# Performance work log

Hardware: AMD Instinct MI355X
Metric: run time of the kernel (lower is better)

## Reference

```python
import jax, jax.numpy as jnp
import numpy as np

B, L, NV = 16, 512, 64
D = 512
PATCH_LEN, STRIDE, PADDING = 16, 8, 8
N_PATCH = (L - PATCH_LEN) // STRIDE + 2  # 64
PRED = 192
MEM = 8192
TOPK = 8
NHEAD = 4
NORM_CONST = 0.4
HEAD_NF = D * N_PATCH


def _pos_emb(n, d):
    pos = np.arange(n)[:, None].astype(np.float32)
    div = np.exp(np.arange(0, d, 2).astype(np.float32) * (-np.log(10000.0) / d))
    pe = np.zeros((n, d), np.float32)
    pe[:, 0::2] = np.sin(pos * div)
    pe[:, 1::2] = np.cos(pos * div)
    return jnp.asarray(pe)

POS = _pos_emb(N_PATCH, D)


def gelu(x):
    return jax.nn.gelu(x, approximate=False)  # torch nn.GELU default = exact erf


def setup_inputs() -> dict:
    key = jax.random.key(0)
    ks = jax.random.split(key, 16)
    s = lambda i, shape, scale=0.02: jax.random.normal(ks[i], shape, jnp.float32) * scale
    return dict(
        x_enc=jax.random.normal(ks[0], (B, L, NV), jnp.float32),
        W_val=s(1, (PATCH_LEN, D), 0.05),
        mem_bank=s(2, (MEM, D), 1.0),
        W_m1=s(3, (D, 2 * D)), b_m1=jnp.zeros((2 * D,), jnp.float32),
        W_m2=s(4, (2 * D, D)), b_m2=jnp.zeros((D,), jnp.float32),
        W_q=s(5, (D, D)), b_q=jnp.zeros((D,), jnp.float32),
        W_k=s(6, (D, D)), b_k=jnp.zeros((D,), jnp.float32),
        W_v=s(7, (D, D)), b_v=jnp.zeros((D,), jnp.float32),
        W_o=s(8, (D, D)), b_o=jnp.zeros((D,), jnp.float32),
        W_g1=s(9, (2 * D, D)), b_g1=jnp.zeros((D,), jnp.float32),
        W_g2=s(10, (D, 2)), b_g2=jnp.zeros((2,), jnp.float32),
        W_h=s(11, (HEAD_NF, PRED)), b_h=jnp.zeros((PRED,), jnp.float32),
        W_f1=s(12, (PRED, 2 * PRED)), b_f1=jnp.zeros((2 * PRED,), jnp.float32),
        W_f2=s(13, (2 * PRED, PRED)), b_f2=jnp.zeros((PRED,), jnp.float32),
    )


def reference(x_enc, W_val, mem_bank, W_m1, b_m1, W_m2, b_m2,
              W_q, b_q, W_k, b_k, W_v, b_v, W_o, b_o,
              W_g1, b_g1, W_g2, b_g2, W_h, b_h, W_f1, b_f1, W_f2, b_f2):
    # instance normalization over the time axis (means detached in torch)
    means = jax.lax.stop_gradient(jnp.mean(x_enc, axis=1, keepdims=True))
    xc = x_enc - means
    stdev = jnp.sqrt(jnp.var(xc, axis=1, keepdims=True) + 1e-5) / NORM_CONST
    x = xc / stdev                                              # [B, L, NV]

    # patch embedding: replication pad at end, unfold, linear + sinusoidal pos
    xt = jnp.transpose(x, (0, 2, 1))                            # [B, NV, L]
    xt = jnp.concatenate([xt, jnp.repeat(xt[..., -1:], PADDING, axis=-1)], axis=-1)
    win = (jnp.arange(N_PATCH) * STRIDE)[:, None] + jnp.arange(PATCH_LEN)  # [N, P]
    patches = xt[..., win].reshape(B * NV, N_PATCH, PATCH_LEN)  # [BN, N, P]
    emb = patches @ W_val + POS                                 # [BN, N, D]

    # local memory: mean-pooled query -> matmul similarity -> top-k gather -> MLP
    qflat = jnp.mean(emb, axis=1)                               # [BN, D]
    sim = qflat @ mem_bank.T                                    # [BN, MEM]
    _, idx = jax.lax.top_k(sim, TOPK)                           # [BN, K]
    retr = mem_bank[idx]                                        # [BN, K, D]
    h = gelu(retr @ W_m1 + b_m1) @ W_m2 + b_m2
    local = jnp.mean(h, axis=1, keepdims=True) + emb            # [BN, N, D]

    # global memory: multihead self-attention (4 heads, batch_first)
    dh = D // NHEAD
    heads = lambda t: t.reshape(B * NV, N_PATCH, NHEAD, dh).transpose(0, 2, 1, 3)
    q = heads(emb @ W_q + b_q)
    k = heads(emb @ W_k + b_k)
    v = heads(emb @ W_v + b_v)
    att = jax.nn.softmax(jnp.einsum('bhqd,bhkd->bhqk', q, k) / jnp.sqrt(jnp.float32(dh)), axis=-1)
    glob = jnp.einsum('bhqk,bhkd->bhqd', att, v).transpose(0, 2, 1, 3).reshape(B * NV, N_PATCH, D)
    glob = glob @ W_o + b_o                                     # [BN, N, D]

    # gated fusion of local/global memory
    comb = jnp.concatenate([local, glob], axis=-1)              # [BN, N, 2D]
    gate = jax.nn.softmax(gelu(comb @ W_g1 + b_g1) @ W_g2 + b_g2, axis=-1)
    mem = gate[..., 0:1] * local + gate[..., 1:2] * glob        # [BN, N, D]

    # flatten -> memory head -> fusion layer with residual
    flat = mem.reshape(B * NV, HEAD_NF)
    mh = (flat @ W_h + b_h).reshape(B, NV, PRED)
    pred = gelu(gelu(mh @ W_f1 + b_f1) @ W_f2 + b_f2) + mh
    pred = jnp.transpose(pred, (0, 2, 1))                       # [B, PRED, NV]

    # denormalize
    return pred * stdev + means
```

## Files before the change

kernel.cpp:

```cpp
#include <hip/hip_runtime.h>
#include <stdint.h>

#define DEV __device__ __forceinline__

typedef uint16_t u16;
typedef __bf16 bf16x8 __attribute__((ext_vector_type(8)));
typedef float f32x4 __attribute__((ext_vector_type(4)));
typedef u16 u16x8 __attribute__((ext_vector_type(8)));

DEV float bf2f(u16 v) { return __uint_as_float(((uint32_t)v) << 16); }
DEV u16 f2bf(float f) {
  uint32_t u = __float_as_uint(f);
  u += 0x7fffu + ((u >> 16) & 1u);
  return (u16)(u >> 16);
}
DEV float gelu_f(float x) { return 0.5f * x * (1.0f + erff(x * 0.7071067811865475f)); }

DEV void gload_lds16(const u16* g, u16* l) {
  __builtin_amdgcn_global_load_lds(
      (const __attribute__((address_space(1))) void*)g,
      (__attribute__((address_space(3))) void*)l, 16, 0, 0);
}

struct __align__(16) Scratch {
  float POSb[64 * 512];
  float meanv[1024];
  float stdv[1024];
  float mh[1024 * 192];
  int idxB[8192];
  float qflat[1024 * 512];
  float gatel[65536 * 2];
  float bqkv[1536];
  u16 hmeanB[1024 * 512];
  u16 gmeanB[1024 * 1024];
  u16 WqkvT[1536 * 512];
  u16 WoT[512 * 512];
  u16 Wm1T[1024 * 512];
  u16 Wm2T[512 * 1024];
  u16 Wg1T[512 * 1024];
  u16 WhT[256 * 32768];
  u16 memdupB[8192 * 1536];
  u16 embh[65536 * 512];
  u16 locglob[65536 * 1024];
  u16 obuf[65536 * 512];
  u16 qkvb[65536 * 1536];
};
__device__ Scratch g_s;

__global__ __launch_bounds__(256) void zerof_kernel(float* __restrict__ p, int n) {
  int t = blockIdx.x * 256 + threadIdx.x;
  if (t < n) p[t] = 0.f;
}
__global__ __launch_bounds__(256) void zerou8_kernel(u16* __restrict__ p, int n8) {
  int t = blockIdx.x * 256 + threadIdx.x;
  if (t < n8) *(u16x8*)(p + (long)t * 8) = (u16x8)0;
}
__global__ __launch_bounds__(256) void biasqkv_kernel(const float* __restrict__ bq,
                                                      const float* __restrict__ bk,
                                                      const float* __restrict__ bv,
                                                      float* __restrict__ o) {
  int t = blockIdx.x * 256 + threadIdx.x;
  o[t] = t < 512 ? bq[t] : (t < 1024 ? bk[t - 512] : bv[t - 1024]);
}

__global__ __launch_bounds__(256) void pos_kernel(float* __restrict__ POS) {
  int n = blockIdx.x;
  int i = threadIdx.x;
  float div = expf((float)(2 * i) * (-9.210340371976184f / 512.0f));
  float arg = (float)n * div;
  POS[n * 512 + 2 * i] = sinf(arg);
  POS[n * 512 + 2 * i + 1] = cosf(arg);
}

__global__ __launch_bounds__(256) void stats_kernel(const float* __restrict__ x_enc,
                                                    float* __restrict__ meanv,
                                                    float* __restrict__ stdv) {
  int b = blockIdx.x;
  int v = threadIdx.x & 63;
  int g = threadIdx.x >> 6;
  float s = 0.f, s2 = 0.f;
  for (int l = g; l < 512; l += 4) {
    float x = x_enc[((long)b * 512 + l) * 64 + v];
    s += x; s2 += x * x;
  }
  __shared__ float sh[2][4][64];
  sh[0][g][v] = s; sh[1][g][v] = s2;
  __syncthreads();
  if (g == 0) {
    s = sh[0][0][v] + sh[0][1][v] + sh[0][2][v] + sh[0][3][v];
    s2 = sh[1][0][v] + sh[1][1][v] + sh[1][2][v] + sh[1][3][v];
    float mu = s * (1.f / 512.f);
    float var = s2 * (1.f / 512.f) - mu * mu;
    meanv[b * 64 + v] = mu;
    stdv[b * 64 + v] = sqrtf(var + 1e-5f) * 2.5f;
  }
}

__global__ __launch_bounds__(256) void transpose_kernel(const float* __restrict__ in,
                                                        u16* __restrict__ out, int R, int C) {
  __shared__ u16 t[32][33];
  int bx = blockIdx.x * 32;
  int by = blockIdx.y * 32;
  int tx = threadIdx.x & 31, ty = threadIdx.x >> 5;
  for (int i = ty; i < 32; i += 8) t[i][tx] = f2bf(in[(long)(by + i) * C + bx + tx]);
  __syncthreads();
  for (int i = ty; i < 32; i += 8) out[(long)(bx + i) * R + by + tx] = t[tx][i];
}

__global__ __launch_bounds__(256) void emb_kernel(const float* __restrict__ x_enc,
                                                  const float* __restrict__ W_val,
                                                  const float* __restrict__ POS,
                                                  const float* __restrict__ meanv,
                                                  const float* __restrict__ stdv,
                                                  u16* __restrict__ embh,
                                                  u16* __restrict__ qsC) {
  int bn = blockIdx.x;
  int b = bn >> 6, v = bn & 63;
  int tid = threadIdx.x;
  __shared__ __align__(16) float wv[16 * 512];
  __shared__ __align__(16) float pt[64 * 16];
  for (int i = tid; i < 8192; i += 256) wv[i] = W_val[i];
  float mu = meanv[bn];
  float inv = 1.f / stdv[bn];
  for (int i = tid; i < 1024; i += 256) {
    int n = i >> 4, p = i & 15;
    int l = n * 8 + p; if (l > 511) l = 511;
    pt[i] = (x_enc[((long)b * 512 + l) * 64 + v] - mu) * inv;
  }
  __syncthreads();
  float qs0 = 0.f, qs1 = 0.f;
  int d0 = tid, d1 = tid + 256;
  for (int n = 0; n < 64; ++n) {
    float a0 = POS[n * 512 + d0], a1 = POS[n * 512 + d1];
#pragma unroll
    for (int p = 0; p < 16; ++p) {
      float pv = pt[n * 16 + p];
      a0 += pv * wv[p * 512 + d0];
      a1 += pv * wv[p * 512 + d1];
    }
    long base = ((long)bn * 64 + n) * 512;
    embh[base + d0] = f2bf(a0);
    embh[base + d1] = f2bf(a1);
    qs0 += a0; qs1 += a1;
  }
  float q0 = qs0 * (1.f / 64.f), q1 = qs1 * (1.f / 64.f);
  u16 h0 = f2bf(q0), l0 = f2bf(q0 - bf2f(h0));
  u16 h1 = f2bf(q1), l1 = f2bf(q1 - bf2f(h1));
  long qb = (long)bn * 1536;
  qsC[qb + d0] = h0; qsC[qb + 512 + d0] = l0; qsC[qb + 1024 + d0] = h0;
  qsC[qb + d1] = h1; qsC[qb + 512 + d1] = l1; qsC[qb + 1024 + d1] = h1;
}

__global__ __launch_bounds__(256) void memdup_kernel(const float* __restrict__ mb,
                                                     u16* __restrict__ md) {
  int t = blockIdx.x * 256 + threadIdx.x;
  int n = t >> 6, k8 = (t & 63) * 8;
  const float* src = mb + (long)n * 512 + k8;
  u16x8 hi, lo;
#pragma unroll
  for (int z = 0; z < 8; ++z) {
    float m = src[z];
    u16 h = f2bf(m);
    hi[z] = h;
    lo[z] = f2bf(m - bf2f(h));
  }
  long base = (long)n * 1536 + k8;
  *(u16x8*)(md + base) = hi;
  *(u16x8*)(md + base + 512) = hi;
  *(u16x8*)(md + base + 1024) = lo;
}

template <int EPI>
__global__ __launch_bounds__(256) void gemm_db(const u16* __restrict__ Ag,
                                               const u16* __restrict__ Bt,
                                               const float* __restrict__ bias,
                                               void* __restrict__ C,
                                               const float* __restrict__ W_g2,
                                               float* __restrict__ gatel,
                                               int lda, int ldb, int K, int Nreal, int ldc,
                                               int nT, long zstride) {
  __shared__ __align__(16) u16 smem[4 * 128 * 64];
  const int tid = threadIdx.x;
  const int id = blockIdx.x;
  const int xcd = id & 7;
  const int kk = id >> 3;
  const long bm = (long)((kk / nT) * 8 + xcd) * 128;
  const long bnn = (long)(kk % nT) * 128;
  const long koff = (long)blockIdx.z * (long)K;
  const int lane = tid & 63;
  const int w = tid >> 6;
  const int wm = (w & 1) * 64;
  const int wn = (w >> 1) * 64;
  const int r16 = lane & 15;
  const int q4 = lane >> 4;

  f32x4 acc[4][4] = {};

  const u16* ap[4];
  const u16* bp[4];
  int ao[4], bo[4];
#pragma unroll
  for (int j = 0; j < 4; ++j) {
    int cid = (j * 4 + w) * 64 + lane;
    int r = cid >> 3;
    int g = (cid & 7) ^ (r & 7);
    ap[j] = Ag + (bm + r) * lda + koff + g * 8;
    bp[j] = Bt + (bnn + r) * ldb + koff + g * 8;
    ao[j] = cid * 8;
    bo[j] = 8192 + cid * 8;
  }

#pragma unroll
  for (int j = 0; j < 4; ++j) gload_lds16(ap[j], smem + ao[j]);
#pragma unroll
  for (int j = 0; j < 4; ++j) gload_lds16(bp[j], smem + bo[j]);

  const int nsteps = K >> 6;
  for (int s = 0; s < nsteps; ++s) {
    const int cur = s & 1;
    u16* buf = smem + cur * 16384;
    if (s + 1 < nsteps) {
      u16* nb = smem + (cur ^ 1) * 16384;
      const int k1 = (s + 1) << 6;
#pragma unroll
      for (int j = 0; j < 4; ++j) gload_lds16(ap[j] + k1, nb + ao[j]);
#pragma unroll
      for (int j = 0; j < 4; ++j) gload_lds16(bp[j] + k1, nb + bo[j]);
      asm volatile("s_waitcnt vmcnt(8)" ::: "memory");
    } else {
      asm volatile("s_waitcnt vmcnt(0)" ::: "memory");
    }
    __builtin_amdgcn_sched_barrier(0);
    __builtin_amdgcn_s_barrier();
    __builtin_amdgcn_sched_barrier(0);
    u16* As = buf;
    u16* Bs = buf + 8192;
#pragma unroll
    for (int sub = 0; sub < 2; ++sub) {
      const int gg = q4 + sub * 4;
      bf16x8 av[4], bv[4];
#pragma unroll
      for (int i = 0; i < 4; ++i) {
        int r = wm + i * 16 + r16;
        av[i] = *reinterpret_cast<const bf16x8*>(As + (r * 8 + (gg ^ (r & 7))) * 8);
      }
#pragma unroll
      for (int j2 = 0; j2 < 4; ++j2) {
        int r = wn + j2 * 16 + r16;
        bv[j2] = *reinterpret_cast<const bf16x8*>(Bs + (r * 8 + (gg ^ (r & 7))) * 8);
      }
#pragma unroll
      for (int i = 0; i < 4; ++i)
#pragma unroll
        for (int j2 = 0; j2 < 4; ++j2)
          acc[i][j2] = __builtin_amdgcn_mfma_f32_16x16x32_bf16(av[i], bv[j2], acc[i][j2], 0, 0, 0);
    }
    __builtin_amdgcn_sched_barrier(0);
    __builtin_amdgcn_s_barrier();
    __builtin_amdgcn_sched_barrier(0);
  }

  if (EPI == 3) {
    float* Cz = (float*)C + (long)blockIdx.z * zstride;
    float* epf = (float*)smem + w * 2048;
#pragma unroll
    for (int half = 0; half < 2; ++half) {
#pragma unroll
      for (int i = 0; i < 2; ++i)
#pragma unroll
        for (int j = 0; j < 4; ++j)
#pragma unroll
          for (int r = 0; r < 4; ++r)
            epf[(i * 16 + q4 * 4 + r) * 64 + j * 16 + r16] = acc[half * 2 + i][j][r];
      __syncthreads();
#pragma unroll
      for (int v2 = 0; v2 < 8; ++v2) {
        int idx = v2 * 64 + lane;
        int row = idx >> 4, c4 = (idx & 15) * 4;
        f32x4 vec = *(const f32x4*)(epf + row * 64 + c4);
        long grow = bm + wm + half * 32 + row;
        int gcol = (int)bnn + wn + c4;
        if (gcol < Nreal) *(f32x4*)(Cz + grow * (long)ldc + gcol) = vec;
      }
      __syncthreads();
    }
  } else if (EPI == 4) {
    float bcol[4], w0[4], w1[4];
#pragma unroll
    for (int j = 0; j < 4; ++j) {
      int gc = (int)bnn + wn + j * 16 + r16;
      bcol[j] = bias[gc];
      w0[j] = W_g2[gc * 2];
      w1[j] = W_g2[gc * 2 + 1];
    }
#pragma unroll
    for (int i = 0; i < 4; ++i)
#pragma unroll
      for (int r = 0; r < 4; ++r) {
        float a0 = 0.f, a1 = 0.f;
#pragma unroll
        for (int j = 0; j < 4; ++j) {
          float h = gelu_f(acc[i][j][r] + bcol[j]);
          a0 += h * w0[j];
          a1 += h * w1[j];
        }
#pragma unroll
        for (int off = 1; off < 16; off <<= 1) {
          a0 += __shfl_xor(a0, off);
          a1 += __shfl_xor(a1, off);
        }
        if (r16 == 0) {
          long row = bm + wm + i * 16 + q4 * 4 + r;
          atomicAdd(&gatel[row * 2], a0);
          atomicAdd(&gatel[row * 2 + 1], a1);
        }
      }
  } else {
    u16* ep = smem + w * 2304;
    float bcol[4];
#pragma unroll
    for (int j = 0; j < 4; ++j) bcol[j] = bias[bnn + wn + j * 16 + r16];
#pragma unroll
    for (int half = 0; half < 2; ++half) {
#pragma unroll
      for (int i = 0; i < 2; ++i)
#pragma unroll
        for (int j = 0; j < 4; ++j)
#pragma unroll
          for (int r = 0; r < 4; ++r) {
            float v = acc[half * 2 + i][j][r] + bcol[j];
            if (EPI == 1) v = gelu_f(v);
            ep[(i * 16 + q4 * 4 + r) * 72 + j * 16 + r16] = f2bf(v);
          }
      __syncthreads();
#pragma unroll
      for (int v2 = 0; v2 < 4; ++v2) {
        int row = v2 * 8 + (lane >> 3);
        int c8 = (lane & 7) * 8;
        u16x8 vec = *(const u16x8*)(ep + row * 72 + c8);
        long grow = bm + wm + half * 32 + row;
        int gcol = (int)bnn + wn + c8;
        if (gcol < Nreal) *(u16x8*)((u16*)C + grow * (long)ldc + gcol) = vec;
      }
      __syncthreads();
    }
  }
}

DEV bool better(float v1, int i1, float v2, int i2) {
  return v1 > v2 || (v1 == v2 && i1 < i2);
}
__global__ __launch_bounds__(256) void topk_kernel(const float* __restrict__ sim,
                                                   int* __restrict__ idxout) {
  const int bn = blockIdx.x;
  const int tid = threadIdx.x;
  const float* row = sim + (long)bn * 8192;
  float bv[8]; int bi[8];
#pragma unroll
  for (int r = 0; r < 8; ++r) { bv[r] = -3.0e38f; bi[r] = 0x7fffffff; }
  for (int n = tid; n < 8192; n += 256) {
    float v = row[n];
    if (better(v, n, bv[7], bi[7])) {
      bv[7] = v; bi[7] = n;
      for (int r = 7; r > 0; --r) {
        if (!better(bv[r], bi[r], bv[r - 1], bi[r - 1])) break;
        float tv = bv[r]; bv[r] = bv[r - 1]; bv[r - 1] = tv;
        int ti = bi[r]; bi[r] = bi[r - 1]; bi[r - 1] = ti;
      }
    }
  }
  __shared__ float lv[256 * 8];
  __shared__ int li[256 * 8];
#pragma unroll
  for (int r = 0; r < 8; ++r) { lv[tid * 8 + r] = bv[r]; li[tid * 8 + r] = bi[r]; }
  __syncthreads();
  for (int step = 128; step >= 1; step >>= 1) {
    if (tid < step) {
      float av[8], xv[8]; int ai[8], xi[8];
#pragma unroll
      for (int r = 0; r < 8; ++r) {
        av[r] = lv[tid * 8 + r]; ai[r] = li[tid * 8 + r];
        xv[r] = lv[(tid + step) * 8 + r]; xi[r] = li[(tid + step) * 8 + r];
      }
      int ia = 0, ib = 0;
      float mv[8]; int mi[8];
#pragma unroll
      for (int r = 0; r < 8; ++r) {
        if (better(av[ia], ai[ia], xv[ib], xi[ib])) { mv[r] = av[ia]; mi[r] = ai[ia]; ++ia; }
        else { mv[r] = xv[ib]; mi[r] = xi[ib]; ++ib; }
      }
#pragma unroll
      for (int r = 0; r < 8; ++r) { lv[tid * 8 + r] = mv[r]; li[tid * 8 + r] = mi[r]; }
    }
    __syncthreads();
  }
  if (tid < 8) idxout[bn * 8 + tid] = li[tid];
}

__global__ __launch_bounds__(256) void gather_kernel(const float* __restrict__ mb,
                                                     const int* __restrict__ idx,
                                                     u16* __restrict__ retrB) {
  int t = blockIdx.x * 256 + threadIdx.x;
  int m = t >> 6;
  int c8 = (t & 63) * 8;
  long r = idx[m];
  if (r < 0) r = 0;
  if (r > 8191) r = 8191;
  const float* src = mb + r * 512 + c8;
  u16x8 o;
#pragma unroll
  for (int z = 0; z < 8; ++z) o[z] = f2bf(src[z]);
  *(u16x8*)(retrB + (long)m * 512 + c8) = o;
}

__global__ __launch_bounds__(256) void gmean_kernel(const u16* __restrict__ hid,
                                                    u16* __restrict__ gmeanB) {
  int t = blockIdx.x * 256 + threadIdx.x;
  int bn = t >> 7, j8 = (t & 127) * 8;
  float s[8] = {};
#pragma unroll
  for (int k = 0; k < 8; ++k) {
    u16x8 v = *(const u16x8*)(hid + (long)(bn * 8 + k) * 1024 + j8);
#pragma unroll
    for (int z = 0; z < 8; ++z) s[z] += bf2f(v[z]);
  }
  u16x8 o;
#pragma unroll
  for (int z = 0; z < 8; ++z) o[z] = f2bf(s[z] * 0.125f);
  *(u16x8*)(gmeanB + (long)bn * 1024 + j8) = o;
}

__global__ __launch_bounds__(256) void attn_kernel(const u16* __restrict__ qkvb,
                                                   u16* __restrict__ obuf) {
  __shared__ __align__(16) u16 smem[26752];
  u16* Qs = smem;
  u16* Ks = smem + 8704;
  float* ss = (float*)(smem + 8704);
  u16* ps = smem;
  u16* Os = smem;
  u16* Vb = smem + 17408;
  float* red = (float*)(smem + 25728);
  const int bn = blockIdx.x, h = blockIdx.y;
  const int tid = threadIdx.x;
  const int lane = tid & 63, w = tid >> 6;
  const int r16 = lane & 15, q4 = lane >> 4;
  const long base = (long)bn * 64 * 1536 + h * 128;

  for (int c = tid; c < 1024; c += 256) {
    int r = c >> 4, c8 = (c & 15) * 8;
    u16x8 vq = *(const u16x8*)(qkvb + base + (long)r * 1536 + c8);
    u16x8 vk = *(const u16x8*)(qkvb + base + (long)r * 1536 + 512 + c8);
    u16x8 vv = *(const u16x8*)(qkvb + base + (long)r * 1536 + 1024 + c8);
    *(u16x8*)(Qs + r * 136 + c8) = vq;
    *(u16x8*)(Ks + r * 136 + c8) = vk;
    int kt = r >> 5, q4t = (r >> 3) & 3, e = r & 7;
    int nt = c8 >> 4, rb = c8 & 15;
    int vbase = (nt * 2 + kt) * 520 + (q4t * 16 + rb) * 8 + e;
#pragma unroll
    for (int z = 0; z < 8; ++z) Vb[vbase + z * 8] = vv[z];
  }
  __syncthreads();

  const int m0 = w * 16;
  f32x4 accS[4] = {};
#pragma unroll
  for (int k0 = 0; k0 < 128; k0 += 32) {
    bf16x8 av = *(const bf16x8*)(Qs + (m0 + r16) * 136 + k0 + q4 * 8);
#pragma unroll
    for (int j = 0; j < 4; ++j) {
      bf16x8 bvf = *(const bf16x8*)(Ks + (j * 16 + r16) * 136 + k0 + q4 * 8);
      accS[j] = __builtin_amdgcn_mfma_f32_16x16x32_bf16(av, bvf, accS[j], 0, 0, 0);
    }
  }
  __syncthreads();
  const float scale = 0.08838834764831845f;
#pragma unroll
  for (int j = 0; j < 4; ++j)
#pragma unroll
    for (int r = 0; r < 4; ++r)
      ss[(m0 + q4 * 4 + r) * 66 + j * 16 + r16] = accS[j][r] * scale;
  __syncthreads();

  {
    int r = tid >> 2, p = tid & 3;
    float* row = ss + r * 66 + p * 16;
    float mx = -3.0e38f;
#pragma unroll
    for (int c2 = 0; c2 < 16; ++c2) mx = fmaxf(mx, row[c2]);
    red[r * 4 + p] = mx;
    __syncthreads();
    float m4 = fmaxf(fmaxf(red[r * 4], red[r * 4 + 1]),
                     fmaxf(red[r * 4 + 2], red[r * 4 + 3]));
    float s = 0.f;
#pragma unroll
    for (int c2 = 0; c2 < 16; ++c2) {
      float e = expf(row[c2] - m4);
      row[c2] = e;
      s += e;
    }
    red[256 + r * 4 + p] = s;
    __syncthreads();
    float inv = 1.f / (red[256 + r * 4] + red[256 + r * 4 + 1] +
                       red[256 + r * 4 + 2] + red[256 + r * 4 + 3]);
    u16x8 o0, o1;
#pragma unroll
    for (int z = 0; z < 8; ++z) {
      o0[z] = f2bf(row[z] * inv);
      o1[z] = f2bf(row[8 + z] * inv);
    }
    *(u16x8*)(ps + r * 72 + p * 16) = o0;
    *(u16x8*)(ps + r * 72 + p * 16 + 8) = o1;
  }
  __syncthreads();

  bf16x8 av0 = *(const bf16x8*)(ps + (m0 + r16) * 72 + q4 * 8);
  bf16x8 av1 = *(const bf16x8*)(ps + (m0 + r16) * 72 + 32 + q4 * 8);
  __syncthreads();
#pragma unroll
  for (int nt = 0; nt < 8; ++nt) {
    f32x4 accO = {};
    bf16x8 bv0 = *(const bf16x8*)(Vb + (nt * 2 + 0) * 520 + lane * 8);
    bf16x8 bv1 = *(const bf16x8*)(Vb + (nt * 2 + 1) * 520 + lane * 8);
    accO = __builtin_amdgcn_mfma_f32_16x16x32_bf16(av0, bv0, accO, 0, 0, 0);
    accO = __builtin_amdgcn_mfma_f32_16x16x32_bf16(av1, bv1, accO, 0, 0, 0);
#pragma unroll
    for (int r = 0; r < 4; ++r) {
      int i = m0 + q4 * 4 + r;
      int col = nt * 16 + r16;
      Os[i * 128 + (col ^ (q4 << 4))] = f2bf(accO[r]);
    }
  }
  __syncthreads();
#pragma unroll
  for (int z = 0; z < 4; ++z) {
    int idx = z * 256 + tid;
    int row = idx >> 4, c8 = (idx & 15) * 8;
    int c8s = c8 ^ (((row >> 2) & 3) << 4);
    u16x8 vec = *(const u16x8*)(Os + row * 128 + c8s);
    *(u16x8*)(obuf + ((long)bn * 64 + row) * 512 + h * 128 + c8) = vec;
  }
}

__global__ __launch_bounds__(256) void local_kernel(const u16* __restrict__ embh,
                                                    const u16* __restrict__ hmeanB,
                                                    u16* __restrict__ locglob) {
  long t = (long)blockIdx.x * 256 + threadIdx.x;
  long e8 = t * 8;
  long m = e8 >> 9;
  int d = (int)(e8 & 511);
  int bn = (int)(m >> 6);
  u16x8 a = *(const u16x8*)(embh + e8);
  u16x8 b = *(const u16x8*)(hmeanB + (long)bn * 512 + d);
  u16x8 o;
#pragma unroll
  for (int z = 0; z < 8; ++z) o[z] = f2bf(bf2f(a[z]) + bf2f(b[z]));
  *(u16x8*)(locglob + m * 1024 + d) = o;
}

__global__ __launch_bounds__(256) void memc_kernel(u16* __restrict__ embh,
                                                   const u16* __restrict__ locglob,
                                                   const float* __restrict__ gatel,
                                                   const float* __restrict__ b_g2) {
  long t = (long)blockIdx.x * 256 + threadIdx.x;
  long e8 = t * 8;
  long m = e8 >> 9;
  int d = (int)(e8 & 511);
  float l0 = gatel[m * 2] + b_g2[0];
  float l1 = gatel[m * 2 + 1] + b_g2[1];
  float mx = fmaxf(l0, l1);
  float e0 = expf(l0 - mx), e1 = expf(l1 - mx);
  float inv = 1.f / (e0 + e1);
  float g0 = e0 * inv, g1 = e1 * inv;
  u16x8 loc = *(const u16x8*)(locglob + m * 1024 + d);
  u16x8 gl = *(const u16x8*)(locglob + m * 1024 + 512 + d);
  u16x8 o;
#pragma unroll
  for (int z = 0; z < 8; ++z) o[z] = f2bf(g0 * bf2f(loc[z]) + g1 * bf2f(gl[z]));
  *(u16x8*)(embh + e8) = o;
}

__global__ __launch_bounds__(256) void fusion_kernel(const float* __restrict__ mh16,
                                                     const float* __restrict__ b_h,
                                                     const float* __restrict__ W_f1,
                                                     const float* __restrict__ b_f1,
                                                     const float* __restrict__ W_f2,
                                                     const float* __restrict__ b_f2,
                                                     const float* __restrict__ meanv,
                                                     const float* __restrict__ stdv,
                                                     float* __restrict__ out) {
  int bn = blockIdx.x;
  int tid = threadIdx.x;
  __shared__ float mrow[192];
  __shared__ float h1[384];
  if (tid < 192) {
    float a = b_h[tid];
#pragma unroll
    for (int z = 0; z < 16; ++z) a += mh16[(long)z * 196608 + (long)bn * 192 + tid];
    mrow[tid] = a;
  }
  __syncthreads();
  for (int j = tid; j < 384; j += 256) {
    float a = b_f1[j];
    for (int i = 0; i < 192; ++i) a += mrow[i] * W_f1[i * 384 + j];
    h1[j] = gelu_f(a);
  }
  __syncthreads();
  if (tid < 192) {
    float a = b_f2[tid];
    for (int j = 0; j < 384; ++j) a += h1[j] * W_f2[j * 192 + tid];
    float o = gelu_f(a) + mrow[tid];
    int b = bn >> 6, v = bn & 63;
    out[((long)b * 192 + tid) * 64 + v] = o * stdv[bn] + meanv[bn];
  }
}

extern "C" void kernel_launch(void* const* d_in, const int* in_sizes, int n_in,
                              void* d_out, int out_size, void* d_ws, size_t ws_size,
                              hipStream_t stream) {
  (void)in_sizes; (void)n_in; (void)out_size; (void)d_ws; (void)ws_size;
  const float* x_enc = (const float*)d_in[0];
  const float* W_val = (const float*)d_in[1];
  const float* mem_bank = (const float*)d_in[2];
  const float* W_m1 = (const float*)d_in[3];
  const float* b_m1 = (const float*)d_in[4];
  const float* W_m2 = (const float*)d_in[5];
  const float* b_m2 = (const float*)d_in[6];
  const float* W_q = (const float*)d_in[7];
  const float* b_q = (const float*)d_in[8];
  const float* W_k = (const float*)d_in[9];
  const float* b_k = (const float*)d_in[10];
  const float* W_v = (const float*)d_in[11];
  const float* b_v = (const float*)d_in[12];
  const float* W_o = (const float*)d_in[13];
  const float* b_o = (const float*)d_in[14];
  const float* W_g1 = (const float*)d_in[15];
  const float* b_g1 = (const float*)d_in[16];
  const float* W_g2 = (const float*)d_in[17];
  const float* b_g2 = (const float*)d_in[18];
  const float* W_h = (const float*)d_in[19];
  const float* b_h = (const float*)d_in[20];
  const float* W_f1 = (const float*)d_in[21];
  const float* b_f1 = (const float*)d_in[22];
  const float* W_f2 = (const float*)d_in[23];
  const float* b_f2 = (const float*)d_in[24];

  void* sp = nullptr;
  hipGetSymbolAddress(&sp, HIP_SYMBOL(g_s));
  Scratch* S = (Scratch*)sp;
  float* simB = (float*)S->qkvb;
  u16* qsC = S->qkvb + (size_t)16 * 1024 * 1024;
  u16* retrB = S->qkvb + (size_t)18 * 1024 * 1024;
  u16* hiddenB = S->qkvb + (size_t)24 * 1024 * 1024;
  float* mh16 = (float*)S->qkvb;

  pos_kernel<<<64, 256, 0, stream>>>(S->POSb);
  stats_kernel<<<16, 256, 0, stream>>>(x_enc, S->meanv, S->stdv);
  zerof_kernel<<<512, 256, 0, stream>>>(S->gatel, 65536 * 2);
  zerou8_kernel<<<1024, 256, 0, stream>>>(S->WhT + (size_t)192 * 32768, 64 * 32768 / 8);
  biasqkv_kernel<<<6, 256, 0, stream>>>(b_q, b_k, b_v, S->bqkv);
  transpose_kernel<<<dim3(16, 16), 256, 0, stream>>>(W_q, S->WqkvT, 512, 512);
  transpose_kernel<<<dim3(16, 16), 256, 0, stream>>>(W_k, S->WqkvT + 512 * 512, 512, 512);
  transpose_kernel<<<dim3(16, 16), 256, 0, stream>>>(W_v, S->WqkvT + 2 * 512 * 512, 512, 512);
  transpose_kernel<<<dim3(16, 16), 256, 0, stream>>>(W_o, S->WoT, 512, 512);
  transpose_kernel<<<dim3(32, 16), 256, 0, stream>>>(W_m1, S->Wm1T, 512, 1024);
  transpose_kernel<<<dim3(16, 32), 256, 0, stream>>>(W_m2, S->Wm2T, 1024, 512);
  transpose_kernel<<<dim3(16, 32), 256, 0, stream>>>(W_g1, S->Wg1T, 1024, 512);
  transpose_kernel<<<dim3(6, 1024), 256, 0, stream>>>(W_h, S->WhT, 32768, 192);
  memdup_kernel<<<2048, 256, 0, stream>>>(mem_bank, S->memdupB);

  emb_kernel<<<1024, 256, 0, stream>>>(x_enc, W_val, S->POSb, S->meanv, S->stdv,
                                       S->embh, qsC);
  gemm_db<3><<<512, 256, 0, stream>>>(qsC, S->memdupB, nullptr, simB, nullptr, nullptr,
                                      1536, 1536, 1536, 8192, 8192, 64, 0L);
  topk_kernel<<<1024, 256, 0, stream>>>(simB, S->idxB);
  gather_kernel<<<2048, 256, 0, stream>>>(mem_bank, S->idxB, retrB);
  gemm_db<1><<<512, 256, 0, stream>>>(retrB, S->Wm1T, b_m1, hiddenB, nullptr, nullptr,
                                      512, 512, 512, 1024, 1024, 8, 0L);
  gmean_kernel<<<512, 256, 0, stream>>>(hiddenB, S->gmeanB);
  gemm_db<0><<<32, 256, 0, stream>>>(S->gmeanB, S->Wm2T, b_m2, S->hmeanB, nullptr, nullptr,
                                     1024, 1024, 1024, 512, 512, 4, 0L);
  gemm_db<0><<<6144, 256, 0, stream>>>(S->embh, S->WqkvT, S->bqkv, S->qkvb, nullptr, nullptr,
                                       512, 512, 512, 1536, 1536, 12, 0L);
  local_kernel<<<16384, 256, 0, stream>>>(S->embh, S->hmeanB, S->locglob);
  attn_kernel<<<dim3(1024, 4), 256, 0, stream>>>(S->qkvb, S->obuf);
  gemm_db<0><<<2048, 256, 0, stream>>>(S->obuf, S->WoT, b_o, S->locglob + 512, nullptr, nullptr,
                                       512, 512, 512, 512, 1024, 4, 0L);
  gemm_db<4><<<2048, 256, 0, stream>>>(S->locglob, S->Wg1T, b_g1, nullptr,
                                       W_g2, S->gatel, 1024, 1024, 1024, 512, 0, 4, 0L);
  memc_kernel<<<16384, 256, 0, stream>>>(S->embh, S->locglob, S->gatel, b_g2);
  gemm_db<3><<<dim3(16, 1, 16), 256, 0, stream>>>(S->embh, S->WhT, nullptr, mh16,
                                                  nullptr, nullptr,
                                                  32768, 32768, 2048, 192, 192, 2,
                                                  196608L);
  fusion_kernel<<<1024, 256, 0, stream>>>(mh16, b_h, W_f1, b_f1, W_f2, b_f2,
                                          S->meanv, S->stdv, (float*)d_out);
}
```

Before: 933.9 us.

## Merge prep kernels, fuse gather into topk, split-K mem MLP and head GEMMs

Folds the fifteen small setup launches (positional table, stats, zeroing, bias packing, weight transposes, memory-bank split) into one block-indexed prep kernel, cutting launch overhead and letting the pieces run concurrently. The retrieved-row gather now happens at the end of topk, removing a separate kernel and the index round trip. The 1024x512 mem MLP second GEMM becomes a 4-way split-K writing fp32 partials that local_kernel sums with the bias, so this tiny GEMM occupies more CUs. The head GEMM's split-K count rises from 16 to 32, trading more partial-sum reads in fusion_kernel for more parallel blocks.

```diff
diff --git a/kernel.cpp b/kernel.cpp
--- a/kernel.cpp
+++ b/kernel.cpp
@@ -26,12 +26,9 @@
   float POSb[64 * 512];
   float meanv[1024];
   float stdv[1024];
-  float mh[1024 * 192];
   int idxB[8192];
-  float qflat[1024 * 512];
   float gatel[65536 * 2];
   float bqkv[1536];
-  u16 hmeanB[1024 * 512];
   u16 gmeanB[1024 * 1024];
   u16 WqkvT[1536 * 512];
   u16 WoT[512 * 512];
@@ -47,64 +44,90 @@
 };
 __device__ Scratch g_s;
 
-__global__ __launch_bounds__(256) void zerof_kernel(float* __restrict__ p, int n) {
-  int t = blockIdx.x * 256 + threadIdx.x;
-  if (t < n) p[t] = 0.f;
-}
-__global__ __launch_bounds__(256) void zerou8_kernel(u16* __restrict__ p, int n8) {
-  int t = blockIdx.x * 256 + threadIdx.x;
-  if (t < n8) *(u16x8*)(p + (long)t * 8) = (u16x8)0;
-}
-__global__ __launch_bounds__(256) void biasqkv_kernel(const float* __restrict__ bq,
-                                                      const float* __restrict__ bk,
-                                                      const float* __restrict__ bv,
-                                                      float* __restrict__ o) {
-  int t = blockIdx.x * 256 + threadIdx.x;
-  o[t] = t < 512 ? bq[t] : (t < 1024 ? bk[t - 512] : bv[t - 1024]);
-}
-
-__global__ __launch_bounds__(256) void pos_kernel(float* __restrict__ POS) {
-  int n = blockIdx.x;
-  int i = threadIdx.x;
-  float div = expf((float)(2 * i) * (-9.210340371976184f / 512.0f));
-  float arg = (float)n * div;
-  POS[n * 512 + 2 * i] = sinf(arg);
-  POS[n * 512 + 2 * i + 1] = cosf(arg);
-}
-
-__global__ __launch_bounds__(256) void stats_kernel(const float* __restrict__ x_enc,
-                                                    float* __restrict__ meanv,
-                                                    float* __restrict__ stdv) {
-  int b = blockIdx.x;
-  int v = threadIdx.x & 63;
-  int g = threadIdx.x >> 6;
-  float s = 0.f, s2 = 0.f;
-  for (int l = g; l < 512; l += 4) {
-    float x = x_enc[((long)b * 512 + l) * 64 + v];
-    s += x; s2 += x * x;
-  }
+__global__ __launch_bounds__(256) void prep_kernel(const float* __restrict__ x_enc,
+                                                   const float* __restrict__ bq,
+                                                   const float* __restrict__ bk,
+                                                   const float* __restrict__ bv,
+                                                   const float* __restrict__ W_q,
+                                                   const float* __restrict__ W_k,
+                                                   const float* __restrict__ W_v,
+                                                   const float* __restrict__ W_o,
+                                                   const float* __restrict__ W_m1,
+                                                   const float* __restrict__ W_m2,
+                                                   const float* __restrict__ W_g1,
+                                                   const float* __restrict__ W_h,
+                                                   const float* __restrict__ mem_bank) {
+  Scratch* S = &g_s;
+  const int id = blockIdx.x;
+  const int tid = threadIdx.x;
+  __shared__ u16 tsh[32][33];
   __shared__ float sh[2][4][64];
-  sh[0][g][v] = s; sh[1][g][v] = s2;
-  __syncthreads();
-  if (g == 0) {
-    s = sh[0][0][v] + sh[0][1][v] + sh[0][2][v] + sh[0][3][v];
-    s2 = sh[1][0][v] + sh[1][1][v] + sh[1][2][v] + sh[1][3][v];
-    float mu = s * (1.f / 512.f);
-    float var = s2 * (1.f / 512.f) - mu * mu;
-    meanv[b * 64 + v] = mu;
-    stdv[b * 64 + v] = sqrtf(var + 1e-5f) * 2.5f;
-  }
-}
-
-__global__ __launch_bounds__(256) void transpose_kernel(const float* __restrict__ in,
-                                                        u16* __restrict__ out, int R, int C) {
-  __shared__ u16 t[32][33];
-  int bx = blockIdx.x * 32;
-  int by = blockIdx.y * 32;
-  int tx = threadIdx.x & 31, ty = threadIdx.x >> 5;
-  for (int i = ty; i < 32; i += 8) t[i][tx] = f2bf(in[(long)(by + i) * C + bx + tx]);
-  __syncthreads();
-  for (int i = ty; i < 32; i += 8) out[(long)(bx + i) * R + by + tx] = t[tx][i];
+
+  if (id < 64) {
+    int n = id, i = tid;
+    float div = expf((float)(2 * i) * (-9.210340371976184f / 512.0f));
+    float arg = (float)n * div;
+    S->POSb[n * 512 + 2 * i] = sinf(arg);
+    S->POSb[n * 512 + 2 * i + 1] = cosf(arg);
+  } else if (id < 80) {
+    int b = id - 64;
+    int v = tid & 63, g = tid >> 6;
+    float s = 0.f, s2 = 0.f;
+    for (int l = g; l < 512; l += 4) {
+      float x = x_enc[((long)b * 512 + l) * 64 + v];
+      s += x; s2 += x * x;
+    }
+    sh[0][g][v] = s; sh[1][g][v] = s2;
+    __syncthreads();
+    if (g == 0) {
+      s = sh[0][0][v] + sh[0][1][v] + sh[0][2][v] + sh[0][3][v];
+      s2 = sh[1][0][v] + sh[1][1][v] + sh[1][2][v] + sh[1][3][v];
+      float mu = s * (1.f / 512.f);
+      float var = s2 * (1.f / 512.f) - mu * mu;
+      S->meanv[b * 64 + v] = mu;
+      S->stdv[b * 64 + v] = sqrtf(var + 1e-5f) * 2.5f;
+    }
+  } else if (id < 592) {
+    int t = (id - 80) * 256 + tid;
+    S->gatel[t] = 0.f;
+  } else if (id < 1616) {
+    int t = (id - 592) * 256 + tid;
+    *(u16x8*)(S->WhT + (size_t)192 * 32768 + (long)t * 8) = (u16x8)0;
+  } else if (id < 1622) {
+    int t = (id - 1616) * 256 + tid;
+    S->bqkv[t] = t < 512 ? bq[t] : (t < 1024 ? bk[t - 512] : bv[t - 1024]);
+  } else if (id < 10326) {
+    int i = id - 1622;
+    const float* tin; u16* tout; int R, C, bx, by;
+    if (i < 256)       { tin = W_q;  tout = S->WqkvT;             R = 512;   C = 512;  bx = (i & 15) * 32; by = (i >> 4) * 32; }
+    else if (i < 512)  { i -= 256;  tin = W_k;  tout = S->WqkvT + 512 * 512;     R = 512;   C = 512;  bx = (i & 15) * 32; by = (i >> 4) * 32; }
+    else if (i < 768)  { i -= 512;  tin = W_v;  tout = S->WqkvT + 2 * 512 * 512; R = 512;   C = 512;  bx = (i & 15) * 32; by = (i >> 4) * 32; }
+    else if (i < 1024) { i -= 768;  tin = W_o;  tout = S->WoT;    R = 512;   C = 512;  bx = (i & 15) * 32; by = (i >> 4) * 32; }
+    else if (i < 1536) { i -= 1024; tin = W_m1; tout = S->Wm1T;   R = 512;   C = 1024; bx = (i & 31) * 32; by = (i >> 5) * 32; }
+    else if (i < 2048) { i -= 1536; tin = W_m2; tout = S->Wm2T;   R = 1024;  C = 512;  bx = (i & 15) * 32; by = (i >> 4) * 32; }
+    else if (i < 2560) { i -= 2048; tin = W_g1; tout = S->Wg1T;   R = 1024;  C = 512;  bx = (i & 15) * 32; by = (i >> 4) * 32; }
+    else               { i -= 2560; tin = W_h;  tout = S->WhT;    R = 32768; C = 192;  bx = (i % 6) * 32;  by = (i / 6) * 32; }
+    int tx = tid & 31, ty = tid >> 5;
+    for (int r = ty; r < 32; r += 8) tsh[r][tx] = f2bf(tin[(long)(by + r) * C + bx + tx]);
+    __syncthreads();
+    for (int r = ty; r < 32; r += 8) tout[(long)(bx + r) * R + by + tx] = tsh[tx][r];
+  } else {
+    int t = (id - 10326) * 256 + tid;
+    int n = t >> 6, k8 = (t & 63) * 8;
+    const float* src = mem_bank + (long)n * 512 + k8;
+    u16x8 hi, lo;
+#pragma unroll
+    for (int z = 0; z < 8; ++z) {
+      float m = src[z];
+      u16 h = f2bf(m);
+      hi[z] = h;
+      lo[z] = f2bf(m - bf2f(h));
+    }
+    long base = (long)n * 1536 + k8;
+    *(u16x8*)(S->memdupB + base) = hi;
+    *(u16x8*)(S->memdupB + base + 512) = hi;
+    *(u16x8*)(S->memdupB + base + 1024) = lo;
+  }
 }
 
 __global__ __launch_bounds__(256) void emb_kernel(const float* __restrict__ x_enc,
@@ -149,25 +172,6 @@
   long qb = (long)bn * 1536;
   qsC[qb + d0] = h0; qsC[qb + 512 + d0] = l0; qsC[qb + 1024 + d0] = h0;
   qsC[qb + d1] = h1; qsC[qb + 512 + d1] = l1; qsC[qb + 1024 + d1] = h1;
-}
-
-__global__ __launch_bounds__(256) void memdup_kernel(const float* __restrict__ mb,
-                                                     u16* __restrict__ md) {
-  int t = blockIdx.x * 256 + threadIdx.x;
-  int n = t >> 6, k8 = (t & 63) * 8;
-  const float* src = mb + (long)n * 512 + k8;
-  u16x8 hi, lo;
-#pragma unroll
-  for (int z = 0; z < 8; ++z) {
-    float m = src[z];
-    u16 h = f2bf(m);
-    hi[z] = h;
-    lo[z] = f2bf(m - bf2f(h));
-  }
-  long base = (long)n * 1536 + k8;
-  *(u16x8*)(md + base) = hi;
-  *(u16x8*)(md + base + 512) = hi;
-  *(u16x8*)(md + base + 1024) = lo;
 }
 
 template <int EPI>
@@ -351,7 +355,9 @@
   return v1 > v2 || (v1 == v2 && i1 < i2);
 }
 __global__ __launch_bounds__(256) void topk_kernel(const float* __restrict__ sim,
-                                                   int* __restrict__ idxout) {
+                                                   int* __restrict__ idxout,
+                                                   const float* __restrict__ mb,
+                                                   u16* __restrict__ retrB) {
   const int bn = blockIdx.x;
   const int tid = threadIdx.x;
   const float* row = sim + (long)bn * 8192;
@@ -395,22 +401,17 @@
     __syncthreads();
   }
   if (tid < 8) idxout[bn * 8 + tid] = li[tid];
-}
-
-__global__ __launch_bounds__(256) void gather_kernel(const float* __restrict__ mb,
-                                                     const int* __restrict__ idx,
-                                                     u16* __restrict__ retrB) {
-  int t = blockIdx.x * 256 + threadIdx.x;
-  int m = t >> 6;
-  int c8 = (t & 63) * 8;
-  long r = idx[m];
-  if (r < 0) r = 0;
-  if (r > 8191) r = 8191;
-  const float* src = mb + r * 512 + c8;
-  u16x8 o;
-#pragma unroll
-  for (int z = 0; z < 8; ++z) o[z] = f2bf(src[z]);
-  *(u16x8*)(retrB + (long)m * 512 + c8) = o;
+  for (int e = tid; e < 512; e += 256) {
+    int rr = e >> 6, c8 = (e & 63) * 8;
+    long r = li[rr];
+    if (r < 0) r = 0;
+    if (r > 8191) r = 8191;
+    const float* src = mb + r * 512 + c8;
+    u16x8 o;
+#pragma unroll
+    for (int z = 0; z < 8; ++z) o[z] = f2bf(src[z]);
+    *(u16x8*)(retrB + ((long)bn * 8 + rr) * 512 + c8) = o;
+  }
 }
 
 __global__ __launch_bounds__(256) void gmean_kernel(const u16* __restrict__ hid,
@@ -542,7 +543,8 @@
 }
 
 __global__ __launch_bounds__(256) void local_kernel(const u16* __restrict__ embh,
-                                                    const u16* __restrict__ hmeanB,
+                                                    const float* __restrict__ hs,
+                                                    const float* __restrict__ b_m2,
                                                     u16* __restrict__ locglob) {
   long t = (long)blockIdx.x * 256 + threadIdx.x;
   long e8 = t * 8;
@@ -550,10 +552,18 @@
   int d = (int)(e8 & 511);
   int bn = (int)(m >> 6);
   u16x8 a = *(const u16x8*)(embh + e8);
-  u16x8 b = *(const u16x8*)(hmeanB + (long)bn * 512 + d);
+  float h[8];
+#pragma unroll
+  for (int z = 0; z < 8; ++z) h[z] = b_m2[d + z];
+#pragma unroll
+  for (int zz = 0; zz < 4; ++zz) {
+    const float* sp = hs + (long)zz * 524288 + (long)bn * 512 + d;
+#pragma unroll
+    for (int z = 0; z < 8; ++z) h[z] += sp[z];
+  }
   u16x8 o;
 #pragma unroll
-  for (int z = 0; z < 8; ++z) o[z] = f2bf(bf2f(a[z]) + bf2f(b[z]));
+  for (int z = 0; z < 8; ++z) o[z] = f2bf(bf2f(a[z]) + h[z]);
   *(u16x8*)(locglob + m * 1024 + d) = o;
 }
 
@@ -579,7 +589,7 @@
   *(u16x8*)(embh + e8) = o;
 }
 
-__global__ __launch_bounds__(256) void fusion_kernel(const float* __restrict__ mh16,
+__global__ __launch_bounds__(256) void fusion_kernel(const float* __restrict__ mh32,
                                                      const float* __restrict__ b_h,
                                                      const float* __restrict__ W_f1,
                                                      const float* __restrict__ b_f1,
@@ -595,7 +605,7 @@
   if (tid < 192) {
     float a = b_h[tid];
 #pragma unroll
-    for (int z = 0; z < 16; ++z) a += mh16[(long)z * 196608 + (long)bn * 192 + tid];
+    for (int z = 0; z < 32; ++z) a += mh32[(long)z * 196608 + (long)bn * 192 + tid];
     mrow[tid] = a;
   }
   __syncthreads();
@@ -651,47 +661,35 @@
   u16* qsC = S->qkvb + (size_t)16 * 1024 * 1024;
   u16* retrB = S->qkvb + (size_t)18 * 1024 * 1024;
   u16* hiddenB = S->qkvb + (size_t)24 * 1024 * 1024;
-  float* mh16 = (float*)S->qkvb;
-
-  pos_kernel<<<64, 256, 0, stream>>>(S->POSb);
-  stats_kernel<<<16, 256, 0, stream>>>(x_enc, S->meanv, S->stdv);
-  zerof_kernel<<<512, 256, 0, stream>>>(S->gatel, 65536 * 2);
-  zerou8_kernel<<<1024, 256, 0, stream>>>(S->WhT + (size_t)192 * 32768, 64 * 32768 / 8);
-  biasqkv_kernel<<<6, 256, 0, stream>>>(b_q, b_k, b_v, S->bqkv);
-  transpose_kernel<<<dim3(16, 16), 256, 0, stream>>>(W_q, S->WqkvT, 512, 512);
-  transpose_kernel<<<dim3(16, 16), 256, 0, stream>>>(W_k, S->WqkvT + 512 * 512, 512, 512);
-  transpose_kernel<<<dim3(16, 16), 256, 0, stream>>>(W_v, S->WqkvT + 2 * 512 * 512, 512, 512);
-  transpose_kernel<<<dim3(16, 16), 256, 0, stream>>>(W_o, S->WoT, 512, 512);
-  transpose_kernel<<<dim3(32, 16), 256, 0, stream>>>(W_m1, S->Wm1T, 512, 1024);
-  transpose_kernel<<<dim3(16, 32), 256, 0, stream>>>(W_m2, S->Wm2T, 1024, 512);
-  transpose_kernel<<<dim3(16, 32), 256, 0, stream>>>(W_g1, S->Wg1T, 1024, 512);
-  transpose_kernel<<<dim3(6, 1024), 256, 0, stream>>>(W_h, S->WhT, 32768, 192);
-  memdup_kernel<<<2048, 256, 0, stream>>>(mem_bank, S->memdupB);
-
+  float* mh32 = (float*)S->qkvb;
+  float* hs = (float*)S->obuf;
+
+  prep_kernel<<<12374, 256, 0, stream>>>(x_enc, b_q, b_k, b_v, W_q, W_k, W_v, W_o,
+                                         W_m1, W_m2, W_g1, W_h, mem_bank);
   emb_kernel<<<1024, 256, 0, stream>>>(x_enc, W_val, S->POSb, S->meanv, S->stdv,
                                        S->embh, qsC);
   gemm_db<3><<<512, 256, 0, stream>>>(qsC, S->memdupB, nullptr, simB, nullptr, nullptr,
                                       1536, 1536, 1536, 8192, 8192, 64, 0L);
-  topk_kernel<<<1024, 256, 0, stream>>>(simB, S->idxB);
-  gather_kernel<<<2048, 256, 0, stream>>>(mem_bank, S->idxB, retrB);
+  topk_kernel<<<1024, 256, 0, stream>>>(simB, S->idxB, mem_bank, retrB);
   gemm_db<1><<<512, 256, 0, stream>>>(retrB, S->Wm1T, b_m1, hiddenB, nullptr, nullptr,
                                       512, 512, 512, 1024, 1024, 8, 0L);
   gmean_kernel<<<512, 256, 0, stream>>>(hiddenB, S->gmeanB);
-  gemm_db<0><<<32, 256, 0, stream>>>(S->gmeanB, S->Wm2T, b_m2, S->hmeanB, nullptr, nullptr,
-                                     1024, 1024, 1024, 512, 512, 4, 0L);
+  gemm_db<3><<<dim3(32, 1, 4), 256, 0, stream>>>(S->gmeanB, S->Wm2T, nullptr, hs,
+                                                 nullptr, nullptr,
+                                                 1024, 1024, 256, 512, 512, 4, 524288L);
   gemm_db<0><<<6144, 256, 0, stream>>>(S->embh, S->WqkvT, S->bqkv, S->qkvb, nullptr, nullptr,
                                        512, 512, 512, 1536, 1536, 12, 0L);
-  local_kernel<<<16384, 256, 0, stream>>>(S->embh, S->hmeanB, S->locglob);
+  local_kernel<<<16384, 256, 0, stream>>>(S->embh, hs, b_m2, S->locglob);
   attn_kernel<<<dim3(1024, 4), 256, 0, stream>>>(S->qkvb, S->obuf);
   gemm_db<0><<<2048, 256, 0, stream>>>(S->obuf, S->WoT, b_o, S->locglob + 512, nullptr, nullptr,
                                        512, 512, 512, 512, 1024, 4, 0L);
   gemm_db<4><<<2048, 256, 0, stream>>>(S->locglob, S->Wg1T, b_g1, nullptr,
                                        W_g2, S->gatel, 1024, 1024, 1024, 512, 0, 4, 0L);
   memc_kernel<<<16384, 256, 0, stream>>>(S->embh, S->locglob, S->gatel, b_g2);
-  gemm_db<3><<<dim3(16, 1, 16), 256, 0, stream>>>(S->embh, S->WhT, nullptr, mh16,
+  gemm_db<3><<<dim3(16, 1, 32), 256, 0, stream>>>(S->embh, S->WhT, nullptr, mh32,
                                                   nullptr, nullptr,
-                                                  32768, 32768, 2048, 192, 192, 2,
+                                                  32768, 32768, 1024, 192, 192, 2,
                                                   196608L);
-  fusion_kernel<<<1024, 256, 0, stream>>>(mh16, b_h, W_f1, b_f1, W_f2, b_f2,
+  fusion_kernel<<<1024, 256, 0, stream>>>(mh32, b_h, W_f1, b_f1, W_f2, b_f2,
                                           S->meanv, S->stdv, (float*)d_out);
 }
```

Measured after the change: 1.014 ms. +8.6%, slower.
